# Kernel tuning notes

Hardware: AMD Instinct MI355X
Metric: run time of the kernel (lower is better)

## Reference

```python
import jax, jax.numpy as jnp
import numpy as np

N = 10000
NEG_SLOPE = 0.2

def _glorot(key, shape):
    fan = shape[0] + shape[-1]
    return jax.random.normal(key, shape, dtype=jnp.float32) * jnp.sqrt(2.0 / fan)

def gat_conv(x, src, dst, W, a_src, a_dst, b, heads, ch, concat, n):
    # PyG GATConv: linear (no bias), per-head attention logits, softmax over
    # incoming edges of each target node, weighted scatter-sum, final bias.
    h = (x @ W).reshape(n, heads, ch)                     # [N,H,C]
    al_s = jnp.einsum('nhc,hc->nh', h, a_src)             # [N,H]
    al_d = jnp.einsum('nhc,hc->nh', h, a_dst)
    e = jax.nn.leaky_relu(al_s[src] + al_d[dst], NEG_SLOPE)  # [E,H]
    emax = jax.ops.segment_max(e, dst, num_segments=n)    # [N,H]
    emax = jnp.where(jnp.isfinite(emax), emax, 0.0)
    p = jnp.exp(e - emax[dst])
    denom = jax.ops.segment_sum(p, dst, num_segments=n)   # [N,H]
    alpha = p / (denom[dst] + 1e-16)                      # [E,H]
    out = jax.ops.segment_sum(h[src] * alpha[:, :, None], dst, num_segments=n)
    out = out.reshape(n, heads * ch) if concat else out.mean(axis=1)
    return out + b

def _with_self_loops(edge_index, n):
    loop = jnp.arange(n, dtype=edge_index.dtype)
    src = jnp.concatenate([edge_index[0], loop])
    dst = jnp.concatenate([edge_index[1], loop])
    return src, dst

def setup_inputs() -> dict:
    key = jax.random.key(0)
    ks = jax.random.split(key, 20)
    in_dim, out_dim, E = 128, 256, 160000
    x = jax.random.normal(ks[0], (N, in_dim), dtype=jnp.float32)
    edge_index = jax.random.randint(ks[1], (2, E), 0, N, dtype=jnp.int64)
    return {
        'x': x, 'edge_index': edge_index,
        # conv1: GATConv(128, 256, heads=4, concat=True)
        'W1': _glorot(ks[2], (in_dim, 4 * 256)),
        'a1s': _glorot(ks[3], (4, 256)), 'a1d': _glorot(ks[4], (4, 256)),
        'b1': jnp.zeros((1024,), jnp.float32),
        'S1w': _glorot(ks[5], (in_dim, 1024)), 'S1b': jnp.zeros((1024,), jnp.float32),
        # conv2: GATConv(1024, 256, heads=4, concat=True)
        'W2': _glorot(ks[6], (1024, 4 * 256)),
        'a2s': _glorot(ks[7], (4, 256)), 'a2d': _glorot(ks[8], (4, 256)),
        'b2': jnp.zeros((1024,), jnp.float32),
        'S2w': _glorot(ks[9], (1024, 1024)), 'S2b': jnp.zeros((1024,), jnp.float32),
        # conv3: GATConv(1024, 256, heads=6, concat=False)
        'W3': _glorot(ks[10], (1024, 6 * out_dim)),
        'a3s': _glorot(ks[11], (6, out_dim)), 'a3d': _glorot(ks[12], (6, out_dim)),
        'b3': jnp.zeros((out_dim,), jnp.float32),
        'S3w': _glorot(ks[13], (1024, out_dim)), 'S3b': jnp.zeros((out_dim,), jnp.float32),
    }

def reference(x, edge_index, W1, a1s, a1d, b1, S1w, S1b,
              W2, a2s, a2d, b2, S2w, S2b,
              W3, a3s, a3d, b3, S3w, S3b):
    src, dst = _with_self_loops(edge_index, N)
    h = jax.nn.elu(gat_conv(x, src, dst, W1, a1s, a1d, b1, 4, 256, True, N) + x @ S1w + S1b)
    h = jax.nn.elu(gat_conv(h, src, dst, W2, a2s, a2d, b2, 4, 256, True, N) + h @ S2w + S2b)
    out = gat_conv(h, src, dst, W3, a3s, a3d, b3, 6, 256, False, N) + h @ S3w + S3b
    return out
```

## Files before the change

kernel.cpp:

```cpp
#include <hip/hip_runtime.h>
#include <cfloat>
#include <cmath>
#include <cstdint>

#define NN 10000
#define EE 160000
#define ETOT 170000
#define MPAD 10112

typedef _Float16 f16;
typedef __attribute__((ext_vector_type(8))) _Float16 f16x8;
typedef __attribute__((ext_vector_type(4))) float f32x4;

__global__ __launch_bounds__(256) void count_deg_k(const int* __restrict__ ei,
                                                   int* __restrict__ deg) {
    int e = blockIdx.x * 256 + threadIdx.x;
    if (e < ETOT) {
        int dst = (e < EE) ? ei[EE + e] : (e - EE);
        atomicAdd(&deg[dst], 1);
    }
}

__global__ __launch_bounds__(256) void sc1_k(const int* __restrict__ deg,
                                             int* __restrict__ tmp,
                                             int* __restrict__ bsum) {
    __shared__ int s[256];
    int i = blockIdx.x * 256 + threadIdx.x;
    int v = (i < NN) ? deg[i] : 0;
    s[threadIdx.x] = v;
    __syncthreads();
    for (int d = 1; d < 256; d <<= 1) {
        int t = (threadIdx.x >= d) ? s[threadIdx.x - d] : 0;
        __syncthreads();
        s[threadIdx.x] += t;
        __syncthreads();
    }
    if (i < NN) tmp[i] = s[threadIdx.x];
    if (threadIdx.x == 255) bsum[blockIdx.x] = s[255];
}

__global__ __launch_bounds__(64) void sc2_k(const int* __restrict__ bsum,
                                            int* __restrict__ bbase) {
    int lane = threadIdx.x;
    int v = (lane < 40) ? bsum[lane] : 0;
    int incl = v;
    for (int d = 1; d < 64; d <<= 1) {
        int t = __shfl_up(incl, d, 64);
        if (lane >= d) incl += t;
    }
    if (lane < 40) bbase[lane] = incl - v;
}

__global__ __launch_bounds__(256) void sc3_k(const int* __restrict__ deg,
                                             const int* __restrict__ tmp,
                                             const int* __restrict__ bbase,
                                             int* __restrict__ offs,
                                             int* __restrict__ pos) {
    int i = blockIdx.x * 256 + threadIdx.x;
    if (i < NN) {
        int incl = tmp[i] + bbase[blockIdx.x];
        offs[i + 1] = incl;
        pos[i]      = incl - deg[i];
    }
    if (i == 0) offs[0] = 0;
}

__global__ __launch_bounds__(256) void scatter_k(const int* __restrict__ ei,
                                                 int* __restrict__ pos,
                                                 int* __restrict__ esrc) {
    int e = blockIdx.x * 256 + threadIdx.x;
    if (e < ETOT) {
        int dst = (e < EE) ? ei[EE + e] : (e - EE);
        int src = (e < EE) ? ei[e]      : (e - EE);
        int p = atomicAdd(&pos[dst], 1);
        esrc[p] = src;
    }
}

__device__ __forceinline__ int swz(int r, int ko) { return ko ^ ((r >> 1) & 3); }

template <bool DOELU>
__global__ __launch_bounds__(256) void convA_k(const float* __restrict__ A,
                                               f16* __restrict__ hi,
                                               f16* __restrict__ lo,
                                               int M, int K, int kshift) {
    int idx = blockIdx.x * 256 + threadIdx.x;
    int row = idx >> kshift;
    int kc  = idx & ((1 << kshift) - 1);
    float v[8];
    if (row < M) {
        const float* p = A + (size_t)row * K + kc * 8;
        float4 f0 = *(const float4*)p, f1 = *(const float4*)(p + 4);
        v[0]=f0.x; v[1]=f0.y; v[2]=f0.z; v[3]=f0.w;
        v[4]=f1.x; v[5]=f1.y; v[6]=f1.z; v[7]=f1.w;
        if (DOELU) {
#pragma unroll
            for (int i = 0; i < 8; i++) v[i] = (v[i] > 0.f) ? v[i] : expf(v[i]) - 1.f;
        }
    } else {
#pragma unroll
        for (int i = 0; i < 8; i++) v[i] = 0.f;
    }
    int mblk = row >> 7, r = row & 127;
    int kblk = kc >> 2,  ko = kc & 3;
    int KB = K >> 5;
    size_t off = ((size_t)(mblk * KB + kblk)) * 4096 + r * 32 + swz(r, ko) * 8;
    f16x8 h, l;
#pragma unroll
    for (int i = 0; i < 8; i++) {
        f16 hv = (f16)v[i];
        h[i] = hv;
        l[i] = (f16)(v[i] - (float)hv);
    }
    *(f16x8*)(hi + off) = h;
    *(f16x8*)(lo + off) = l;
}

__global__ __launch_bounds__(256) void convB_k(const float* __restrict__ B,
                                               f16* __restrict__ Bdst,
                                               int NcSrc, int colOff, int KB) {
    int n  = blockIdx.x * 256 + threadIdx.x;
    int kc = blockIdx.y;
    const float* p = B + (size_t)(kc * 8) * NcSrc + n;
    int gcol = colOff + n;
    int nblk = gcol >> 7, r = gcol & 127;
    int kblk = kc >> 2,  ko = kc & 3;
    size_t off = ((size_t)(nblk * KB + kblk)) * 4096 + r * 32 + swz(r, ko) * 8;
    f16x8 h;
#pragma unroll
    for (int i = 0; i < 8; i++) h[i] = (f16)p[(size_t)i * NcSrc];
    *(f16x8*)(Bdst + off) = h;
}

__device__ __forceinline__ void gl_lds16(const void* g, void* l) {
    __builtin_amdgcn_global_load_lds(
        (const __attribute__((address_space(1))) uint32_t*)g,
        (__attribute__((address_space(3))) uint32_t*)l, 16, 0, 0);
}

#define MMBUF 24576

__global__ __launch_bounds__(256) void mm_k(const f16* __restrict__ Ahi,
                                            const f16* __restrict__ Alo,
                                            const f16* __restrict__ Bhi,
                                            float* __restrict__ C2,
                                            f16* __restrict__ C1h,
                                            const float* __restrict__ bias1,
                                            const float* __restrict__ bias2,
                                            const float* __restrict__ a_s,
                                            const float* __restrict__ a_d,
                                            float* __restrict__ als,
                                            float* __restrict__ ald,
                                            int M, int KB, int NB1,
                                            int N1, int N2, int H) {
    __shared__ __align__(16) char lds[2 * MMBUF];
    const int tid = threadIdx.x;

    const int nwg  = gridDim.x * gridDim.y;
    const int orig = blockIdx.y * gridDim.x + blockIdx.x;
    const int q = nwg >> 3, rr = nwg & 7;
    const int xcd = orig & 7, rk = orig >> 3;
    const int lin = (xcd < rr ? xcd * (q + 1) : rr * (q + 1) + (xcd - rr) * q) + rk;
    const int mblk = lin / gridDim.x, nblk = lin % gridDim.x;

    const int lane = tid & 63, w = tid >> 6;
    const int wr = w >> 1, wc = w & 1;
    const int kg = lane >> 4, l15 = lane & 15;

    int offA[4], offB[4];
#pragma unroll
    for (int t = 0; t < 4; t++) {
        int ra = wr * 64 + t * 16 + l15;
        offA[t] = ra * 64 + swz(ra, kg) * 16;
        int rb = wc * 64 + t * 16 + l15;
        offB[t] = 16384 + rb * 64 + swz(rb, kg) * 16;
    }

    const char* gAh = (const char*)Ahi + (size_t)mblk * KB * 8192;
    const char* gAl = (const char*)Alo + (size_t)mblk * KB * 8192;
    const char* gBh = (const char*)Bhi + (size_t)nblk * KB * 8192;

    f32x4 acc[4][4];
#pragma unroll
    for (int i = 0; i < 4; i++)
#pragma unroll
        for (int j = 0; j < 4; j++) acc[i][j] = (f32x4){0.f, 0.f, 0.f, 0.f};

    const int t16 = tid * 16;
    auto stage = [&](int kb, int buf) {
        const size_t tk = (size_t)kb * 8192;
        char* l = lds + buf * MMBUF;
        gl_lds16(gAh + tk + t16,        l + t16);
        gl_lds16(gAh + tk + 4096 + t16, l + 4096 + t16);
        gl_lds16(gAl + tk + t16,        l + 8192 + t16);
        gl_lds16(gAl + tk + 4096 + t16, l + 12288 + t16);
        gl_lds16(gBh + tk + t16,        l + 16384 + t16);
        gl_lds16(gBh + tk + 4096 + t16, l + 20480 + t16);
    };

    stage(0, 0);
    __syncthreads();

    for (int kb = 0; kb < KB; kb++) {
        const int cur = kb & 1;
        if (kb + 1 < KB) stage(kb + 1, cur ^ 1);

        const char* l = lds + cur * MMBUF;
        f16x8 ah[4], al[4], b[4];
#pragma unroll
        for (int t = 0; t < 4; t++) {
            ah[t] = *(const f16x8*)(l + offA[t]);
            al[t] = *(const f16x8*)(l + 8192 + offA[t]);
            b[t]  = *(const f16x8*)(l + offB[t]);
        }
#pragma unroll
        for (int i = 0; i < 4; i++)
#pragma unroll
            for (int j = 0; j < 4; j++) {
                acc[i][j] = __builtin_amdgcn_mfma_f32_16x16x32_f16(ah[i], b[j], acc[i][j], 0, 0, 0);
                acc[i][j] = __builtin_amdgcn_mfma_f32_16x16x32_f16(al[i], b[j], acc[i][j], 0, 0, 0);
            }
        __syncthreads();
    }

    const int rowBase = mblk * 128 + wr * 64;
    const int colBase = nblk * 128 + wc * 64;
    if (nblk < NB1) {
#pragma unroll
        for (int i = 0; i < 4; i++)
#pragma unroll
            for (int j = 0; j < 4; j++) {
                int col = colBase + j * 16 + l15;
#pragma unroll
                for (int q2 = 0; q2 < 4; q2++) {
                    int row = rowBase + i * 16 + kg * 4 + q2;
                    C1h[(size_t)row * N1 + col] = (f16)acc[i][j][q2];
                }
            }
        const int head = nblk >> 1;
        const int cIn  = (nblk & 1) * 128 + wc * 64;
        float asv[4], adv[4];
#pragma unroll
        for (int j = 0; j < 4; j++) {
            asv[j] = a_s[head * 256 + cIn + j * 16 + l15];
            adv[j] = a_d[head * 256 + cIn + j * 16 + l15];
        }
#pragma unroll
        for (int i = 0; i < 4; i++)
#pragma unroll
            for (int q2 = 0; q2 < 4; q2++) {
                float vs = acc[i][0][q2] * asv[0] + acc[i][1][q2] * asv[1]
                         + acc[i][2][q2] * asv[2] + acc[i][3][q2] * asv[3];
                float vd = acc[i][0][q2] * adv[0] + acc[i][1][q2] * adv[1]
                         + acc[i][2][q2] * adv[2] + acc[i][3][q2] * adv[3];
                vs += __shfl_xor(vs, 1); vs += __shfl_xor(vs, 2);
                vs += __shfl_xor(vs, 4); vs += __shfl_xor(vs, 8);
                vd += __shfl_xor(vd, 1); vd += __shfl_xor(vd, 2);
                vd += __shfl_xor(vd, 4); vd += __shfl_xor(vd, 8);
                if (l15 == 0) {
                    int row = rowBase + i * 16 + kg * 4 + q2;
                    if (row < M) {
                        atomicAdd(&als[row * H + head], vs);
                        atomicAdd(&ald[row * H + head], vd);
                    }
                }
            }
    } else {
        const int cb2 = NB1 * 128;
#pragma unroll
        for (int i = 0; i < 4; i++)
#pragma unroll
            for (int j = 0; j < 4; j++) {
                int c2 = colBase + j * 16 + l15 - cb2;
                float bsum = bias1[c2] + bias2[c2];
#pragma unroll
                for (int q2 = 0; q2 < 4; q2++) {
                    int row = rowBase + i * 16 + kg * 4 + q2;
                    if (row < M) C2[(size_t)row * N2 + c2] = acc[i][j][q2] + bsum;
                }
            }
    }
}

template <int H, bool MEAN>
__global__ __launch_bounds__(256) void smagg_k(const int* __restrict__ offs,
                                               const int* __restrict__ esrc,
                                               const float* __restrict__ als,
                                               const float* __restrict__ ald,
                                               const f16* __restrict__ hfeat16,
                                               const float* __restrict__ skipin,
                                               float* __restrict__ outf,
                                               f16* __restrict__ hiT,
                                               f16* __restrict__ loT) {
    constexpr int NC = H * 256;
    __shared__ float s_l[128 * 9];
    __shared__ float s_p[128 * 9];
    __shared__ int   s_src[128];
    __shared__ float s_m[8], s_s[8], s_scale[8], s_ad[8];

    const int n = blockIdx.x;
    const int tid = threadIdx.x;
    const int base = offs[n], cnt = offs[n + 1] - base;

    if (tid < H) {
        s_m[tid] = -1e30f;
        s_s[tid] = 0.f;
        s_ad[tid] = ald[n * H + tid];
    }
    float acc[H];
#pragma unroll
    for (int h = 0; h < H; h++) acc[h] = 0.f;
    __syncthreads();

    for (int c0 = 0; c0 < cnt; c0 += 128) {
        const int mcnt = min(128, cnt - c0);
        if (tid < mcnt) {
            int src = esrc[base + c0 + tid];
            s_src[tid] = src;
#pragma unroll
            for (int h = 0; h < H; h++) {
                float l = als[src * H + h] + s_ad[h];
                l = (l < 0.f) ? 0.2f * l : l;
                s_l[tid * 9 + h] = l;
            }
        }
        __syncthreads();
        if (tid < H * 32) {
            int h = tid >> 5, l5 = tid & 31;
            float m = -1e30f;
            for (int e = l5; e < mcnt; e += 32) m = fmaxf(m, s_l[e * 9 + h]);
            for (int o = 16; o > 0; o >>= 1) m = fmaxf(m, __shfl_xor(m, o, 32));
            float mNew = fmaxf(s_m[h], m);
            float ssum = 0.f;
            for (int e = l5; e < mcnt; e += 32) ssum += __expf(s_l[e * 9 + h] - mNew);
            for (int o = 16; o > 0; o >>= 1) ssum += __shfl_xor(ssum, o, 32);
            if (l5 == 0) {
                float scale = __expf(s_m[h] - mNew);
                s_scale[h] = scale;
                s_s[h] = s_s[h] * scale + ssum;
                s_m[h] = mNew;
            }
        }
        __syncthreads();
        if (tid < mcnt) {
#pragma unroll
            for (int h = 0; h < H; h++)
                s_p[tid * 9 + h] = __expf(s_l[tid * 9 + h] - s_m[h]);
        }
#pragma unroll
        for (int h = 0; h < H; h++) acc[h] *= s_scale[h];
        __syncthreads();
        for (int e = 0; e < mcnt; e++) {
            const f16* hp = hfeat16 + (size_t)s_src[e] * NC + tid;
#pragma unroll
            for (int h = 0; h < H; h++)
                acc[h] += s_p[e * 9 + h] * (float)hp[h * 256];
        }
        __syncthreads();
    }

    if (MEAN) {
        float v = 0.f;
#pragma unroll
        for (int h = 0; h < H; h++) v += acc[h] / (s_s[h] + 1e-16f);
        outf[(size_t)n * 256 + tid] += v * (1.f / 6.f);
    } else {
        const int mblk = n >> 7, r = n & 127;
#pragma unroll
        for (int h = 0; h < H; h++) {
            int c = h * 256 + tid;
            float v = skipin[(size_t)n * NC + c] + acc[h] / (s_s[h] + 1e-16f);
            v = (v > 0.f) ? v : expf(v) - 1.f;
            f16 hv = (f16)v;
            f16 lv = (f16)(v - (float)hv);
            int kblk = c >> 5, ko = (c >> 3) & 3;
            size_t off = ((size_t)(mblk * 32 + kblk)) * 4096
                       + r * 32 + swz(r, ko) * 8 + (c & 7);
            hiT[off] = hv;
            loT[off] = lv;
        }
    }
}

extern "C" void kernel_launch(void* const* d_in, const int* in_sizes, int n_in,
                              void* d_out, int out_size, void* d_ws, size_t ws_size,
                              hipStream_t stream) {
    const float* x   = (const float*)d_in[0];
    const int*   ei  = (const int*)d_in[1];
    const float* W1  = (const float*)d_in[2];
    const float* a1s = (const float*)d_in[3];
    const float* a1d = (const float*)d_in[4];
    const float* b1  = (const float*)d_in[5];
    const float* S1w = (const float*)d_in[6];
    const float* S1b = (const float*)d_in[7];
    const float* W2  = (const float*)d_in[8];
    const float* a2s = (const float*)d_in[9];
    const float* a2d = (const float*)d_in[10];
    const float* b2  = (const float*)d_in[11];
    const float* S2w = (const float*)d_in[12];
    const float* S2b = (const float*)d_in[13];
    const float* W3  = (const float*)d_in[14];
    const float* a3s = (const float*)d_in[15];
    const float* a3d = (const float*)d_in[16];
    const float* b3  = (const float*)d_in[17];
    const float* S3w = (const float*)d_in[18];
    const float* S3b = (const float*)d_in[19];
    float* out = (float*)d_out;

    float* ws = (float*)d_ws;
    size_t o = 0;
    float* bufA = ws + o; o += (size_t)NN * 1024;
    float* bufB = ws + o; o += (size_t)NN * 1024;
    float* als  = ws + o; o += (size_t)NN * 6;
    float* ald  = ws + o; o += (size_t)NN * 6;
    f16* hfeat16 = (f16*)(ws + o); o += (size_t)MPAD * 1536 / 2;
    f16* AhiT = (f16*)(ws + o); o += (size_t)MPAD * 1024 / 2;
    f16* AloT = (f16*)(ws + o); o += (size_t)MPAD * 1024 / 2;
    f16* Bt1  = (f16*)(ws + o); o += (size_t)16 * 4  * 4096 / 2;
    f16* Bt2  = (f16*)(ws + o); o += (size_t)16 * 32 * 4096 / 2;
    f16* Bt3  = (f16*)(ws + o); o += (size_t)14 * 32 * 4096 / 2;
    int* deg   = (int*)(ws + o);
    int* tmp   = deg + NN;
    int* bsum  = tmp + NN;
    int* bbase = bsum + 64;
    int* offs  = bbase + 64;
    int* pos   = offs + NN + 1;
    int* esrc  = pos + NN;

    hipMemsetAsync(deg, 0, NN * sizeof(int), stream);
    count_deg_k<<<(ETOT + 255) / 256, 256, 0, stream>>>(ei, deg);
    sc1_k<<<40, 256, 0, stream>>>(deg, tmp, bsum);
    sc2_k<<<1, 64, 0, stream>>>(bsum, bbase);
    sc3_k<<<40, 256, 0, stream>>>(deg, tmp, bbase, offs, pos);
    scatter_k<<<(ETOT + 255) / 256, 256, 0, stream>>>(ei, pos, esrc);

    convB_k<<<dim3(4, 16),  256, 0, stream>>>(W1,  Bt1, 1024, 0,    4);
    convB_k<<<dim3(4, 16),  256, 0, stream>>>(S1w, Bt1, 1024, 1024, 4);
    convB_k<<<dim3(4, 128), 256, 0, stream>>>(W2,  Bt2, 1024, 0,    32);
    convB_k<<<dim3(4, 128), 256, 0, stream>>>(S2w, Bt2, 1024, 1024, 32);
    convB_k<<<dim3(6, 128), 256, 0, stream>>>(W3,  Bt3, 1536, 0,    32);
    convB_k<<<dim3(1, 128), 256, 0, stream>>>(S3w, Bt3, 256,  1536, 32);

    convA_k<false><<<MPAD * 16 / 256, 256, 0, stream>>>(x, AhiT, AloT, NN, 128, 4);
    hipMemsetAsync(als, 0, NN * 12 * sizeof(float), stream);
    mm_k<<<dim3(16, 79), 256, 0, stream>>>(AhiT, AloT, Bt1, bufA, hfeat16, S1b, b1,
                                           a1s, a1d, als, ald,
                                           NN, 4, 8, 1024, 1024, 4);
    smagg_k<4, false><<<NN, 256, 0, stream>>>(offs, esrc, als, ald, hfeat16,
                                              bufA, nullptr, AhiT, AloT);

    hipMemsetAsync(als, 0, NN * 12 * sizeof(float), stream);
    mm_k<<<dim3(16, 79), 256, 0, stream>>>(AhiT, AloT, Bt2, bufB, hfeat16, S2b, b2,
                                           a2s, a2d, als, ald,
                                           NN, 32, 8, 1024, 1024, 4);
    smagg_k<4, false><<<NN, 256, 0, stream>>>(offs, esrc, als, ald, hfeat16,
                                              bufB, nullptr, AhiT, AloT);

    hipMemsetAsync(als, 0, NN * 12 * sizeof(float), stream);
    mm_k<<<dim3(14, 79), 256, 0, stream>>>(AhiT, AloT, Bt3, out, hfeat16, S3b, b3,
                                           a3s, a3d, als, ald,
                                           NN, 32, 12, 1536, 256, 6);
    smagg_k<6, true><<<NN, 256, 0, stream>>>(offs, esrc, als, ald, hfeat16,
                                             nullptr, out, nullptr, nullptr);
}
```

Baseline: 553.6 us.

## Map one wavefront per node in softmax-aggregate kernel with vectorized gathers

The aggregation kernel now assigns one 64-lane wavefront per destination node (four nodes per block) instead of a whole 256-thread block per node. Online softmax statistics are computed with wave shuffles rather than shared memory and __syncthreads. Neighbour features are gathered as 16-byte f16x8 loads, and skip inputs and hi/lo outputs use vector loads and stores. This removes block-level barriers and scalar 2-byte gathers, at the cost of more registers per thread and serial per-edge shuffles within each wave.

New measurement: 561.5 us. No clear change (+1.4%).

```diff
diff --git a/kernel.cpp b/kernel.cpp
--- a/kernel.cpp
+++ b/kernel.cpp
@@ -293,92 +293,166 @@
                                                f16* __restrict__ hiT,
                                                f16* __restrict__ loT) {
     constexpr int NC = H * 256;
-    __shared__ float s_l[128 * 9];
-    __shared__ float s_p[128 * 9];
-    __shared__ int   s_src[128];
-    __shared__ float s_m[8], s_s[8], s_scale[8], s_ad[8];
-
-    const int n = blockIdx.x;
-    const int tid = threadIdx.x;
+    const int lane = threadIdx.x & 63;
+    const int n = blockIdx.x * 4 + (threadIdx.x >> 6);
     const int base = offs[n], cnt = offs[n + 1] - base;
 
-    if (tid < H) {
-        s_m[tid] = -1e30f;
-        s_s[tid] = 0.f;
-        s_ad[tid] = ald[n * H + tid];
-    }
-    float acc[H];
-#pragma unroll
-    for (int h = 0; h < H; h++) acc[h] = 0.f;
-    __syncthreads();
-
-    for (int c0 = 0; c0 < cnt; c0 += 128) {
-        const int mcnt = min(128, cnt - c0);
-        if (tid < mcnt) {
-            int src = esrc[base + c0 + tid];
-            s_src[tid] = src;
-#pragma unroll
-            for (int h = 0; h < H; h++) {
-                float l = als[src * H + h] + s_ad[h];
-                l = (l < 0.f) ? 0.2f * l : l;
-                s_l[tid * 9 + h] = l;
-            }
-        }
-        __syncthreads();
-        if (tid < H * 32) {
-            int h = tid >> 5, l5 = tid & 31;
-            float m = -1e30f;
-            for (int e = l5; e < mcnt; e += 32) m = fmaxf(m, s_l[e * 9 + h]);
-            for (int o = 16; o > 0; o >>= 1) m = fmaxf(m, __shfl_xor(m, o, 32));
-            float mNew = fmaxf(s_m[h], m);
-            float ssum = 0.f;
-            for (int e = l5; e < mcnt; e += 32) ssum += __expf(s_l[e * 9 + h] - mNew);
-            for (int o = 16; o > 0; o >>= 1) ssum += __shfl_xor(ssum, o, 32);
-            if (l5 == 0) {
-                float scale = __expf(s_m[h] - mNew);
-                s_scale[h] = scale;
-                s_s[h] = s_s[h] * scale + ssum;
-                s_m[h] = mNew;
-            }
-        }
-        __syncthreads();
-        if (tid < mcnt) {
-#pragma unroll
-            for (int h = 0; h < H; h++)
-                s_p[tid * 9 + h] = __expf(s_l[tid * 9 + h] - s_m[h]);
-        }
-#pragma unroll
-        for (int h = 0; h < H; h++) acc[h] *= s_scale[h];
-        __syncthreads();
+    float ad[H];
+#pragma unroll
+    for (int h = 0; h < H; h++) ad[h] = ald[n * H + h];
+
+    float m[H], ssum[H];
+#pragma unroll
+    for (int h = 0; h < H; h++) { m[h] = -1e30f; ssum[h] = 0.f; }
+
+    float acc4[16];
+    float acc6[3][8];
+    if (H == 4) {
+#pragma unroll
+        for (int i = 0; i < 16; i++) acc4[i] = 0.f;
+    } else {
+#pragma unroll
+        for (int b = 0; b < 3; b++)
+#pragma unroll
+            for (int j = 0; j < 8; j++) acc6[b][j] = 0.f;
+    }
+    const int h0 = lane >> 4;
+    const int par = (lane >= 32) ? 1 : 0;
+
+    for (int c0 = 0; c0 < cnt; c0 += 64) {
+        const int mcnt = min(64, cnt - c0);
+        int src = 0;
+        float l[H];
+        if (lane < mcnt) {
+            src = esrc[base + c0 + lane];
+            if (H == 4) {
+                float4 a4 = *(const float4*)(als + (size_t)src * 4);
+                l[0] = a4.x + ad[0]; l[1] = a4.y + ad[1];
+                l[2] = a4.z + ad[2]; l[3] = a4.w + ad[3];
+            } else {
+                const float2* ap = (const float2*)(als + (size_t)src * 6);
+#pragma unroll
+                for (int b = 0; b < 3; b++) {
+                    float2 a2 = ap[b];
+                    l[2 * b]     = a2.x + ad[2 * b];
+                    l[2 * b + 1] = a2.y + ad[2 * b + 1];
+                }
+            }
+#pragma unroll
+            for (int h = 0; h < H; h++) l[h] = (l[h] < 0.f) ? 0.2f * l[h] : l[h];
+        } else {
+#pragma unroll
+            for (int h = 0; h < H; h++) l[h] = -1e30f;
+        }
+        float sc[H], p[H];
+#pragma unroll
+        for (int h = 0; h < H; h++) {
+            float v = l[h];
+            for (int o = 32; o > 0; o >>= 1) v = fmaxf(v, __shfl_xor(v, o, 64));
+            float mN = fmaxf(m[h], v);
+            sc[h] = __expf(m[h] - mN);
+            m[h] = mN;
+            p[h] = (lane < mcnt) ? __expf(l[h] - mN) : 0.f;
+            float s = p[h];
+            for (int o = 32; o > 0; o >>= 1) s += __shfl_xor(s, o, 64);
+            ssum[h] = ssum[h] * sc[h] + s;
+        }
+        if (H == 4) {
+            float scm = (h0 < 2) ? ((h0 == 0) ? sc[0] : sc[1])
+                                 : ((h0 == 2) ? sc[2] : sc[3]);
+#pragma unroll
+            for (int i = 0; i < 16; i++) acc4[i] *= scm;
+        } else {
+#pragma unroll
+            for (int b = 0; b < 3; b++) {
+                float scm = par ? sc[2 * b + 1] : sc[2 * b];
+#pragma unroll
+                for (int j = 0; j < 8; j++) acc6[b][j] *= scm;
+            }
+        }
         for (int e = 0; e < mcnt; e++) {
-            const f16* hp = hfeat16 + (size_t)s_src[e] * NC + tid;
-#pragma unroll
-            for (int h = 0; h < H; h++)
-                acc[h] += s_p[e * 9 + h] * (float)hp[h * 256];
-        }
-        __syncthreads();
+            int se = __shfl(src, e, 64);
+            if (H == 4) {
+                float pe0 = __shfl(p[0], e, 64), pe1 = __shfl(p[1], e, 64);
+                float pe2 = __shfl(p[2], e, 64), pe3 = __shfl(p[3], e, 64);
+                float ph = (h0 < 2) ? ((h0 == 0) ? pe0 : pe1)
+                                    : ((h0 == 2) ? pe2 : pe3);
+                const f16* hp = hfeat16 + (size_t)se * 1024 + lane * 16;
+                f16x8 v0 = *(const f16x8*)hp;
+                f16x8 v1 = *(const f16x8*)(hp + 8);
+#pragma unroll
+                for (int i = 0; i < 8; i++) {
+                    acc4[i]     += ph * (float)v0[i];
+                    acc4[8 + i] += ph * (float)v1[i];
+                }
+            } else {
+                float pe[6];
+#pragma unroll
+                for (int h = 0; h < 6; h++) pe[h] = __shfl(p[h], e, 64);
+                const f16* hp = hfeat16 + (size_t)se * 1536 + lane * 8;
+#pragma unroll
+                for (int b = 0; b < 3; b++) {
+                    float ph = par ? pe[2 * b + 1] : pe[2 * b];
+                    f16x8 v = *(const f16x8*)(hp + b * 512);
+#pragma unroll
+                    for (int j = 0; j < 8; j++) acc6[b][j] += ph * (float)v[j];
+                }
+            }
+        }
     }
 
     if (MEAN) {
-        float v = 0.f;
-#pragma unroll
-        for (int h = 0; h < H; h++) v += acc[h] / (s_s[h] + 1e-16f);
-        outf[(size_t)n * 256 + tid] += v * (1.f / 6.f);
+        float pt[8];
+#pragma unroll
+        for (int j = 0; j < 8; j++) pt[j] = 0.f;
+#pragma unroll
+        for (int b = 0; b < 3; b++) {
+            float inv = 1.f / (ssum[par ? 2 * b + 1 : 2 * b] + 1e-16f);
+#pragma unroll
+            for (int j = 0; j < 8; j++) pt[j] += acc6[b][j] * inv;
+        }
+#pragma unroll
+        for (int j = 0; j < 8; j++) pt[j] += __shfl_xor(pt[j], 32, 64);
+        if (lane < 32) {
+            float* op = outf + (size_t)n * 256 + lane * 8;
+            float4 o0 = *(float4*)op, o1 = *(float4*)(op + 4);
+            o0.x += pt[0] * (1.f / 6.f); o0.y += pt[1] * (1.f / 6.f);
+            o0.z += pt[2] * (1.f / 6.f); o0.w += pt[3] * (1.f / 6.f);
+            o1.x += pt[4] * (1.f / 6.f); o1.y += pt[5] * (1.f / 6.f);
+            o1.z += pt[6] * (1.f / 6.f); o1.w += pt[7] * (1.f / 6.f);
+            *(float4*)op = o0; *(float4*)(op + 4) = o1;
+        }
     } else {
+        float inv = 1.f / (ssum[(h0 < 2) ? ((h0 == 0) ? 0 : 1)
+                                         : ((h0 == 2) ? 2 : 3)] + 1e-16f);
+        const float* sp = skipin + (size_t)n * 1024 + lane * 16;
+        float v[16];
+#pragma unroll
+        for (int c = 0; c < 4; c++) {
+            float4 sk = *(const float4*)(sp + c * 4);
+            v[c * 4 + 0] = sk.x + acc4[c * 4 + 0] * inv;
+            v[c * 4 + 1] = sk.y + acc4[c * 4 + 1] * inv;
+            v[c * 4 + 2] = sk.z + acc4[c * 4 + 2] * inv;
+            v[c * 4 + 3] = sk.w + acc4[c * 4 + 3] * inv;
+        }
+        f16x8 hv0, lv0, hv1, lv1;
+#pragma unroll
+        for (int i = 0; i < 8; i++) {
+            float e0 = (v[i] > 0.f) ? v[i] : expf(v[i]) - 1.f;
+            float e1 = (v[8 + i] > 0.f) ? v[8 + i] : expf(v[8 + i]) - 1.f;
+            f16 h0f = (f16)e0, h1f = (f16)e1;
+            hv0[i] = h0f; lv0[i] = (f16)(e0 - (float)h0f);
+            hv1[i] = h1f; lv1[i] = (f16)(e1 - (float)h1f);
+        }
         const int mblk = n >> 7, r = n & 127;
-#pragma unroll
-        for (int h = 0; h < H; h++) {
-            int c = h * 256 + tid;
-            float v = skipin[(size_t)n * NC + c] + acc[h] / (s_s[h] + 1e-16f);
-            v = (v > 0.f) ? v : expf(v) - 1.f;
-            f16 hv = (f16)v;
-            f16 lv = (f16)(v - (float)hv);
-            int kblk = c >> 5, ko = (c >> 3) & 3;
-            size_t off = ((size_t)(mblk * 32 + kblk)) * 4096
-                       + r * 32 + swz(r, ko) * 8 + (c & 7);
-            hiT[off] = hv;
-            loT[off] = lv;
-        }
+        const int kblk = lane >> 1, ko0 = (lane & 1) * 2;
+        size_t tb = ((size_t)(mblk * 32 + kblk)) * 4096 + r * 32;
+        size_t off0 = tb + swz(r, ko0) * 8;
+        size_t off1 = tb + swz(r, ko0 + 1) * 8;
+        *(f16x8*)(hiT + off0) = hv0;
+        *(f16x8*)(hiT + off1) = hv1;
+        *(f16x8*)(loT + off0) = lv0;
+        *(f16x8*)(loT + off1) = lv1;
     }
 }
 
@@ -446,20 +520,20 @@
     mm_k<<<dim3(16, 79), 256, 0, stream>>>(AhiT, AloT, Bt1, bufA, hfeat16, S1b, b1,
                                            a1s, a1d, als, ald,
                                            NN, 4, 8, 1024, 1024, 4);
-    smagg_k<4, false><<<NN, 256, 0, stream>>>(offs, esrc, als, ald, hfeat16,
-                                              bufA, nullptr, AhiT, AloT);
+    smagg_k<4, false><<<NN / 4, 256, 0, stream>>>(offs, esrc, als, ald, hfeat16,
+                                                  bufA, nullptr, AhiT, AloT);
 
     hipMemsetAsync(als, 0, NN * 12 * sizeof(float), stream);
     mm_k<<<dim3(16, 79), 256, 0, stream>>>(AhiT, AloT, Bt2, bufB, hfeat16, S2b, b2,
                                            a2s, a2d, als, ald,
                                            NN, 32, 8, 1024, 1024, 4);
-    smagg_k<4, false><<<NN, 256, 0, stream>>>(offs, esrc, als, ald, hfeat16,
-                                              bufB, nullptr, AhiT, AloT);
+    smagg_k<4, false><<<NN / 4, 256, 0, stream>>>(offs, esrc, als, ald, hfeat16,
+                                                  bufB, nullptr, AhiT, AloT);
 
     hipMemsetAsync(als, 0, NN * 12 * sizeof(float), stream);
     mm_k<<<dim3(14, 79), 256, 0, stream>>>(AhiT, AloT, Bt3, out, hfeat16, S3b, b3,
                                            a3s, a3d, als, ald,
                                            NN, 32, 12, 1536, 256, 6);
-    smagg_k<6, true><<<NN, 256, 0, stream>>>(offs, esrc, als, ald, hfeat16,
-                                             nullptr, out, nullptr, nullptr);
-}
+    smagg_k<6, true><<<NN / 4, 256, 0, stream>>>(offs, esrc, als, ald, hfeat16,
+                                                 nullptr, out, nullptr, nullptr);
+}
```
